# Kernel optimization log

Hardware: AMD Instinct MI355X
Metric: run time of the kernel (lower is better)

## Reference

```python
import jax, jax.numpy as jnp
import numpy as np

N_NODES = 100000
N_EDGES = 1600000
N_GRAPHS = 1000
NODES_PER_GRAPH = 100  # batch vector is arange(N)//100: exactly 100 nodes per graph
HID = 32
MAX_Z = 1000
K = 30
D_LAT = HID * 3 + 1  # 97, total_latent_dim


def setup_inputs() -> dict:
    key = jax.random.key(0)
    ks = jax.random.split(key, 24)
    s = 1.0 / np.sqrt(HID)
    inp = {
        "z": jax.random.randint(ks[0], (N_NODES,), 0, MAX_Z, dtype=jnp.int32),
        "edge_index": jax.random.randint(ks[1], (2, N_EDGES), 0, N_NODES, dtype=jnp.int32),
        "batch": (jnp.arange(N_NODES, dtype=jnp.int32) // NODES_PER_GRAPH),
        "edge_weight": jax.random.uniform(ks[2], (N_EDGES,), jnp.float32, 0.1, 1.0),
        "z_emb": jax.random.normal(ks[3], (MAX_Z, HID), jnp.float32) * 0.1,
        # GCNConv stack: [32->32, 32->32, 32->32, 32->1]
        "Wg1": jax.random.normal(ks[4], (HID, HID)) * s,
        "bg1": jnp.zeros((HID,), jnp.float32),
        "Wg2": jax.random.normal(ks[5], (HID, HID)) * s,
        "bg2": jnp.zeros((HID,), jnp.float32),
        "Wg3": jax.random.normal(ks[6], (HID, HID)) * s,
        "bg3": jnp.zeros((HID,), jnp.float32),
        "Wg4": jax.random.normal(ks[7], (HID, 1)) * s,
        "bg4": jnp.zeros((1,), jnp.float32),
        # Conv1d(1, 16, kernel=97, stride=97)
        "Wc1": jax.random.normal(ks[8], (16, D_LAT)) * (1.0 / np.sqrt(D_LAT)),
        "bc1": jnp.zeros((16,), jnp.float32),
        # Conv1d(16, 32, kernel=5, stride=1)
        "Wc2": jax.random.normal(ks[9], (32, 16, 5)) * (1.0 / np.sqrt(16 * 5)),
        "bc2": jnp.zeros((32,), jnp.float32),
        # Linear(352, 128), Linear(128, 1)
        "Wl1": jax.random.normal(ks[10], (352, 128)) * (1.0 / np.sqrt(352)),
        "bl1": jnp.zeros((128,), jnp.float32),
        "Wl2": jax.random.normal(ks[11], (128, 1)) * (1.0 / np.sqrt(128)),
        "bl2": jnp.zeros((1,), jnp.float32),
    }
    return inp


def gcn_conv(x, src, dst, ew, W, b, n):
    # PyG GCNConv: xW, add self-loops (weight 1), sym-normalize, aggregate at dst, + bias
    xw = x @ W
    deg = jax.ops.segment_sum(ew, dst, num_segments=n) + 1.0  # +1 for self loop
    dinv = jnp.where(deg > 0, jax.lax.rsqrt(deg), 0.0)
    norm = dinv[src] * ew * dinv[dst]                          # [E]
    out = jax.ops.segment_sum(norm[:, None] * xw[src], dst, num_segments=n)
    out = out + xw * (dinv * dinv)[:, None]                    # self-loop term
    return out + b


def _forward(z, edge_index, batch, edge_weight, z_emb, Wg1, bg1, Wg2, bg2, Wg3, bg3,
             Wg4, bg4, Wc1, bc1, Wc2, bc2, Wl1, bl1, Wl2, bl2):
    src, dst = edge_index[0], edge_index[1]
    n = z.shape[0]
    x = z_emb[z]                                              # [N, 32]
    xs = []
    h = x
    for W, b in ((Wg1, bg1), (Wg2, bg2), (Wg3, bg3), (Wg4, bg4)):
        h = jnp.tanh(gcn_conv(h, src, dst, edge_weight, W, b, n))
        xs.append(h)
    x = jnp.concatenate(xs, axis=-1)                          # [N, 97]
    # global_sort_pool: batch is uniform (100 nodes/graph) so dense batching is a reshape
    dense = x.reshape(N_GRAPHS, NODES_PER_GRAPH, D_LAT)       # [B, 100, 97]
    idx = jnp.argsort(-dense[:, :, -1], axis=1)[:, :K]        # sort desc by last channel
    top = jnp.take_along_axis(dense, idx[:, :, None], axis=1)  # [B, 30, 97]
    # Conv1d(1,16,97,stride=97) on flattened [B,1,30*97] == per-slot dense layer
    y = jax.nn.relu(jnp.einsum('bkd,cd->bck', top, Wc1) + bc1[None, :, None])  # [B,16,30]
    y = y.reshape(N_GRAPHS, 16, K // 2, 2).max(axis=-1)        # MaxPool1d(2,2) -> [B,16,15]
    y = jax.lax.conv_general_dilated(y, Wc2, (1,), 'VALID',
                                     dimension_numbers=('NCH', 'OIH', 'NCH'))
    y = jax.nn.relu(y + bc2[None, :, None])                    # [B,32,11]
    y = y.reshape(N_GRAPHS, -1)                                # [B,352]
    y = jax.nn.relu(y @ Wl1 + bl1)                             # dropout: eval mode, identity
    return y @ Wl2 + bl2                                       # [B,1]


def reference(z, edge_index, batch, edge_weight, z_emb, Wg1, bg1, Wg2, bg2, Wg3, bg3,
              Wg4, bg4, Wc1, bc1, Wc2, bc2, Wl1, bl1, Wl2, bl2):
    return _forward(z, edge_index, batch, edge_weight, z_emb, Wg1, bg1, Wg2, bg2, Wg3,
                    bg3, Wg4, bg4, Wc1, bc1, Wc2, bc2, Wl1, bl1, Wl2, bl2)
```

## Files before the change

kernel.cpp:

```cpp
#include <hip/hip_runtime.h>

#define HID 32
#define DLAT 97
#define NPG 100
#define TOPK 30
#define BKT_NODES 128
#define BKT_SHIFT 7
#define NBUCK 1024
#define CAPF 2432
#define CHUNK 8192

typedef float f32x4 __attribute__((ext_vector_type(4)));

__device__ __forceinline__ f32x4 gload4(const float* p) {
    f32x4 r;
    asm volatile("global_load_dwordx4 %0, %1, off" : "=v"(r) : "v"(p));
    return r;
}

__global__ __launch_bounds__(512) void binB1_kernel(
    const int* __restrict__ src, const int* __restrict__ dst,
    const float* __restrict__ ew, int* __restrict__ gcursor,
    int2* __restrict__ bedge, int E) {
    __shared__ int hist[NBUCK];
    __shared__ int lcur[NBUCK];
    __shared__ int dcache[CHUNK];
    for (int i = threadIdx.x; i < NBUCK; i += 512) hist[i] = 0;
    __syncthreads();
    int base = blockIdx.x * CHUNK;
    int M = min(E - base, CHUNK);
    for (int i = threadIdx.x; i < M; i += 512) {
        int d = dst[base + i];
        dcache[i] = d;
        atomicAdd(&hist[d >> BKT_SHIFT], 1);
    }
    __syncthreads();
    for (int b = threadIdx.x; b < NBUCK; b += 512) {
        int v = hist[b];
        lcur[b] = b * CAPF + (v ? atomicAdd(&gcursor[b], v) : 0);
    }
    __syncthreads();
    for (int i = threadIdx.x; i < M; i += 512) {
        int d = dcache[i];
        int slot = atomicAdd(&lcur[d >> BKT_SHIFT], 1);
        bedge[slot] = make_int2(src[base + i] | ((d & (BKT_NODES - 1)) << 20),
                                __float_as_int(ew[base + i]));
    }
}

__global__ __launch_bounds__(256) void scan1024_kernel(
    const int* __restrict__ g, int* __restrict__ bstart) {
    __shared__ int sh[256];
    int t = threadIdx.x;
    int t4 = t * 4;
    int a0 = g[t4], a1 = g[t4 + 1], a2 = g[t4 + 2], a3 = g[t4 + 3];
    int tsum = a0 + a1 + a2 + a3;
    sh[t] = tsum;
    __syncthreads();
    for (int off = 1; off < 256; off <<= 1) {
        int tv = (t >= off) ? sh[t - off] : 0;
        __syncthreads();
        sh[t] += tv;
        __syncthreads();
    }
    int e = sh[t] - tsum;
    bstart[t4] = e;
    bstart[t4 + 1] = e + a0;
    bstart[t4 + 2] = e + a0 + a1;
    bstart[t4 + 3] = e + a0 + a1 + a2;
}

__global__ __launch_bounds__(512) void sortlocal3_kernel(
    const int2* __restrict__ bedge, const int* __restrict__ gcursor,
    const int* __restrict__ bstart,
    const int* __restrict__ z, const float* __restrict__ z_emb,
    const float* __restrict__ W1, int2* __restrict__ csr,
    int* __restrict__ row_start, int* __restrict__ row_deg,
    float* __restrict__ dinv, float* __restrict__ xw_a, int N) {
    __shared__ int2 LDSe[CAPF];
    __shared__ int cnt[BKT_NODES];
    __shared__ int sh2[BKT_NODES];
    __shared__ int lc2[BKT_NODES];
    __shared__ int zloc[BKT_NODES];
    __shared__ float wsum[BKT_NODES];
    __shared__ float dloc[BKT_NODES];
    __shared__ float W1L[HID * HID];

    int b = blockIdx.x, t = threadIdx.x;
    for (int i = t; i < HID * HID; i += 512) W1L[i] = W1[i];
    if (t < BKT_NODES) { cnt[t] = 0; wsum[t] = 0.f; }
    __syncthreads();

    const int begOut = bstart[b];
    const int M = gcursor[b];

    for (int i = t; i < M; i += 512) {
        int2 e = bedge[(size_t)b * CAPF + i];
        LDSe[i] = e;
        int nl = (e.x >> 20) & (BKT_NODES - 1);
        atomicAdd(&cnt[nl], 1);
        atomicAdd(&wsum[nl], __int_as_float(e.y));
    }
    __syncthreads();
    int v = 0, excl = 0;
    int n = b * BKT_NODES + t;
    if (t < BKT_NODES) { v = cnt[t]; sh2[t] = v; }
    __syncthreads();
    for (int off = 1; off < BKT_NODES; off <<= 1) {
        int tv = (t >= off && t < BKT_NODES) ? sh2[t - off] : 0;
        __syncthreads();
        if (t < BKT_NODES) sh2[t] += tv;
        __syncthreads();
    }
    if (t < BKT_NODES) {
        excl = sh2[t] - v;
        lc2[t] = excl;
        float di = 1.f / sqrtf(1.f + wsum[t]);
        dloc[t] = di;
        if (n < N) {
            row_start[n] = begOut + excl;
            row_deg[n] = v;
            dinv[n] = di;
            zloc[t] = z[n];
        } else {
            zloc[t] = 0;
        }
    }
    __syncthreads();
    for (int i = t; i < M; i += 512) {
        int2 e = LDSe[i];
        int slot = atomicAdd(&lc2[(e.x >> 20) & (BKT_NODES - 1)], 1);
        csr[begOut + slot] = make_int2(e.x & 0xFFFFF, e.y);
    }
    int lim = min(BKT_NODES, N - b * BKT_NODES);
    if (lim > 0) {
        for (int idx = t; idx < lim * HID; idx += 512) {
            int nl = idx >> 5, f = idx & 31;
            const float* row = z_emb + (size_t)zloc[nl] * HID;
            float s = 0.f;
#pragma unroll
            for (int k = 0; k < HID; ++k) s += row[k] * W1L[k * HID + f];
            xw_a[(size_t)(b * BKT_NODES + nl) * HID + f] = s * dloc[nl];
        }
    }
}

template <int MODE>
__global__ __launch_bounds__(256) void agg32z_kernel(
    const int* __restrict__ row_start, const int* __restrict__ row_deg,
    const int2* __restrict__ csr, const float* __restrict__ xw,
    const float* __restrict__ b, const float* __restrict__ dinv,
    const float* __restrict__ Wn, float* __restrict__ cout,
    float* __restrict__ xw_next, int N) {
    __shared__ float WnL[HID * HID];
    int t = threadIdx.x;
    if (MODE == 0) {
        for (int i = t; i < HID * HID; i += 256) WnL[i] = Wn[i];
    } else {
        if (t < HID) WnL[t] = Wn[t];
    }
    __syncthreads();
    int tid = blockIdx.x * 256 + t;
    int n = tid >> 5;
    if (n >= N) return;
    int lane = t & 31;
    int eq = lane & 3;
    int f4 = lane & 28;
    int beg = row_start[n];
    int deg = row_deg[n];
    float di = dinv[n];
    float selfv = xw[(size_t)n * HID + lane];
    int end = beg + deg;
    float4 acc = make_float4(0.f, 0.f, 0.f, 0.f);
    for (int i = beg; i < end; i += 32) {
        int e = i + lane;
        int2 ce = csr[min(e, end - 1)];
        float we = (e < end) ? __int_as_float(ce.y) : 0.f;
        int ci = ce.x;
        int jmax = min(8, (end - i + 3) >> 2);
        f32x4 x[8];
        float w[8];
#pragma unroll
        for (int j = 0; j < 8; ++j) {
            if (j < jmax) {
                int s = 4 * j + eq;
                int idx = __shfl(ci, s, 32);
                w[j] = __shfl(we, s, 32);
                x[j] = gload4(xw + (size_t)idx * HID + f4);
            }
        }
        asm volatile("s_waitcnt vmcnt(0)" ::: "memory");
        __builtin_amdgcn_sched_barrier(0);
#pragma unroll
        for (int j = 0; j < 8; ++j) {
            if (j < jmax) {
                acc.x += w[j] * x[j].x;
                acc.y += w[j] * x[j].y;
                acc.z += w[j] * x[j].z;
                acc.w += w[j] * x[j].w;
            }
        }
    }
#pragma unroll
    for (int m = 1; m <= 2; m <<= 1) {
        acc.x += __shfl_xor(acc.x, m, 32);
        acc.y += __shfl_xor(acc.y, m, 32);
        acc.z += __shfl_xor(acc.z, m, 32);
        acc.w += __shfl_xor(acc.w, m, 32);
    }
    float s = (eq == 0) ? acc.x : (eq == 1) ? acc.y : (eq == 2) ? acc.z : acc.w;
    float outv = tanhf(di * (s + selfv) + b[lane]);
    cout[(size_t)n * HID + lane] = outv;

    if (MODE == 0) {
        float p = 0.f;
#pragma unroll
        for (int k = 0; k < HID; ++k) {
            float ok = __shfl(outv, k, 32);
            p += ok * WnL[k * HID + lane];
        }
        xw_next[(size_t)n * HID + lane] = p * di;
    } else {
        float p = outv * WnL[lane];
        p += __shfl_xor(p, 16, 32);
        p += __shfl_xor(p, 8, 32);
        p += __shfl_xor(p, 4, 32);
        p += __shfl_xor(p, 2, 32);
        p += __shfl_xor(p, 1, 32);
        if (lane == 0) xw_next[n] = p * di;
    }
}

__global__ __launch_bounds__(256) void topk_head_kernel(
    const int* __restrict__ row_start, const int* __restrict__ row_deg,
    const int2* __restrict__ csr, const float* __restrict__ xw4,
    const float* __restrict__ b4, const float* __restrict__ dinv,
    const float* __restrict__ cblk,
    const float* __restrict__ Wc1, const float* __restrict__ bc1,
    const float* __restrict__ Wc2, const float* __restrict__ bc2,
    const float* __restrict__ Wl1, const float* __restrict__ bl1,
    const float* __restrict__ Wl2, const float* __restrict__ bl2,
    float* __restrict__ out, int N) {
    int g = blockIdx.x;
    int tid = threadIdx.x;
    __shared__ float v[NPG];
    __shared__ int tidx[TOPK];
    __shared__ float tval[TOPK];
    __shared__ float top[TOPK * DLAT];
    __shared__ float Wc1L[16 * DLAT];
    __shared__ float Wc2L[32 * 16 * 5];
    __shared__ float y1[16 * TOPK];
    __shared__ float y2[16 * 15];
    __shared__ float y3[352];
    __shared__ float r[256];

    for (int i = tid; i < 16 * DLAT; i += 256) Wc1L[i] = Wc1[i];
    for (int i = tid; i < 32 * 16 * 5; i += 256) Wc2L[i] = Wc2[i];

    if (tid < NPG) {
        int n = g * NPG + tid;
        int beg = row_start[n], end = beg + row_deg[n];
        float s0 = 0.f, s1 = 0.f;
        for (int i = beg; i < end; i += 4) {
            int2 e0 = csr[min(i, end - 1)];
            int2 e1 = csr[min(i + 1, end - 1)];
            int2 e2 = csr[min(i + 2, end - 1)];
            int2 e3 = csr[min(i + 3, end - 1)];
            float x0 = xw4[e0.x], x1 = xw4[e1.x], x2 = xw4[e2.x], x3 = xw4[e3.x];
            s0 += __int_as_float(e0.y) * x0;
            if (i + 1 < end) s1 += __int_as_float(e1.y) * x1;
            if (i + 2 < end) s0 += __int_as_float(e2.y) * x2;
            if (i + 3 < end) s1 += __int_as_float(e3.y) * x3;
        }
        v[tid] = tanhf(dinv[n] * ((s0 + s1) + xw4[n]) + b4[0]);
    }
    __syncthreads();
    if (tid < NPG) {
        float vi = v[tid];
        int cnt = 0;
#pragma unroll 4
        for (int j = 0; j < NPG; ++j) {
            float vj = v[j];
            cnt += (vj > vi) || (vj == vi && j < tid);
        }
        if (cnt < TOPK) {
            tidx[cnt] = g * NPG + tid;
            tval[cnt] = vi;
        }
    }
    __syncthreads();

    for (int idx = tid; idx < TOPK * 24; idx += 256) {
        int k = idx / 24, q = idx - k * 24;
        int l = q >> 3, fq = q & 7;
        const float4 val =
            *(const float4*)(cblk + (size_t)l * N * HID + (size_t)tidx[k] * HID + fq * 4);
        float* dst = top + k * DLAT + l * HID + fq * 4;
        dst[0] = val.x; dst[1] = val.y; dst[2] = val.z; dst[3] = val.w;
    }
    if (tid < TOPK) top[tid * DLAT + 96] = tval[tid];
    __syncthreads();

    for (int idx = tid; idx < 16 * TOPK; idx += 256) {
        int c = idx / TOPK, k = idx % TOPK;
        float s = bc1[c];
        const float* w = Wc1L + c * DLAT;
        const float* t = top + k * DLAT;
#pragma unroll 4
        for (int d = 0; d < DLAT; ++d) s += t[d] * w[d];
        y1[c * TOPK + k] = fmaxf(s, 0.f);
    }
    __syncthreads();

    for (int idx = tid; idx < 16 * 15; idx += 256) {
        int c = idx / 15, j = idx % 15;
        y2[idx] = fmaxf(y1[c * TOPK + 2 * j], y1[c * TOPK + 2 * j + 1]);
    }
    __syncthreads();

    for (int idx = tid; idx < 352; idx += 256) {
        int o = idx / 11, t = idx % 11;
        float s = bc2[o];
#pragma unroll
        for (int i = 0; i < 16; ++i) {
#pragma unroll
            for (int k = 0; k < 5; ++k)
                s += Wc2L[(o * 16 + i) * 5 + k] * y2[i * 15 + t + k];
        }
        y3[idx] = fmaxf(s, 0.f);
    }
    __syncthreads();

    {
        int half = tid >> 7;
        int o = tid & 127;
        int d0 = half * 176;
        float s = (half == 0) ? bl1[o] : 0.f;
#pragma unroll 1
        for (int d = d0; d < d0 + 176; d += 8) {
            float wv[8], yv[8];
#pragma unroll
            for (int j = 0; j < 8; ++j) wv[j] = Wl1[(d + j) * 128 + o];
#pragma unroll
            for (int j = 0; j < 8; ++j) yv[j] = y3[d + j];
#pragma unroll
            for (int j = 0; j < 8; ++j) s += yv[j] * wv[j];
        }
        r[tid] = s;
    }
    __syncthreads();
    if (tid < 128) r[tid] = fmaxf(r[tid] + r[tid + 128], 0.f) * Wl2[tid];
    __syncthreads();
    if (tid < 64) r[tid] += r[tid + 64];
    __syncthreads();
    if (tid == 0) {
        float s = 0.f;
        for (int j = 0; j < 64; ++j) s += r[j];
        out[g] = s + bl2[0];
    }
}


extern "C" void kernel_launch(void* const* d_in, const int* in_sizes, int n_in,
                              void* d_out, int out_size, void* d_ws, size_t ws_size,
                              hipStream_t stream) {
    const int* z = (const int*)d_in[0];
    const int* ei = (const int*)d_in[1];
    const float* ew = (const float*)d_in[3];
    const float* z_emb = (const float*)d_in[4];
    const float* Wg[4] = {(const float*)d_in[5], (const float*)d_in[7],
                          (const float*)d_in[9], (const float*)d_in[11]};
    const float* bg[4] = {(const float*)d_in[6], (const float*)d_in[8],
                          (const float*)d_in[10], (const float*)d_in[12]};
    const float* Wc1 = (const float*)d_in[13];
    const float* bc1 = (const float*)d_in[14];
    const float* Wc2 = (const float*)d_in[15];
    const float* bc2 = (const float*)d_in[16];
    const float* Wl1 = (const float*)d_in[17];
    const float* bl1 = (const float*)d_in[18];
    const float* Wl2 = (const float*)d_in[19];
    const float* bl2 = (const float*)d_in[20];
    float* out = (float*)d_out;

    const int N = in_sizes[0];
    const int E = in_sizes[1] / 2;
    const int G = out_size;
    const int* src = ei;
    const int* dst = ei + E;

    auto cdiv = [](long long a, long long b) { return (int)((a + b - 1) / b); };
    const int NB = cdiv(E, CHUNK);
    const int NBKT = cdiv(N, BKT_NODES);

    char* ws = (char*)d_ws;
    int2* bedge = (int2*)ws;                  ws += sizeof(int2) * (size_t)NBUCK * CAPF;
    int2* csr = (int2*)ws;                    ws += sizeof(int2) * (size_t)E;
    int* gcursor = (int*)ws;                  ws += sizeof(int) * NBUCK;
    int* bstart = (int*)ws;                   ws += sizeof(int) * NBUCK;
    int* row_start = (int*)ws;                ws += sizeof(int) * N;
    int* row_deg = (int*)ws;                  ws += sizeof(int) * N;
    float* dinv = (float*)ws;                 ws += sizeof(float) * N;
    float* xw_a = (float*)ws;                 ws += sizeof(float) * (size_t)N * HID;
    float* cblk = (float*)ws;                 ws += sizeof(float) * (size_t)3 * N * HID;
    float* xw4 = (float*)ws;                  ws += sizeof(float) * N;
    float* xw_b = (float*)bedge;
    float* cb0 = cblk;
    float* cb1 = cblk + (size_t)N * HID;
    float* cb2 = cblk + (size_t)2 * N * HID;

    hipMemsetAsync(gcursor, 0, sizeof(int) * NBUCK, stream);
    binB1_kernel<<<NB, 512, 0, stream>>>(src, dst, ew, gcursor, bedge, E);
    scan1024_kernel<<<1, 256, 0, stream>>>(gcursor, bstart);
    sortlocal3_kernel<<<NBKT, 512, 0, stream>>>(bedge, gcursor, bstart, z, z_emb, Wg[0],
                                                csr, row_start, row_deg, dinv, xw_a, N);

    const int AGGB = cdiv((long long)N * 32, 256);
    agg32z_kernel<0><<<AGGB, 256, 0, stream>>>(row_start, row_deg, csr, xw_a, bg[0],
                                               dinv, Wg[1], cb0, xw_b, N);
    agg32z_kernel<0><<<AGGB, 256, 0, stream>>>(row_start, row_deg, csr, xw_b, bg[1],
                                               dinv, Wg[2], cb1, xw_a, N);
    agg32z_kernel<1><<<AGGB, 256, 0, stream>>>(row_start, row_deg, csr, xw_a, bg[2],
                                               dinv, Wg[3], cb2, xw4, N);

    topk_head_kernel<<<G, 256, 0, stream>>>(row_start, row_deg, csr, xw4, bg[3], dinv,
                                            cblk, Wc1, bc1, Wc2, bc2, Wl1, bl1,
                                            Wl2, bl2, out, N);
}
```

Baseline: 346.8 us.

## Replace bucketed two-pass CSR build with per-node histogram and atomic scatter

The CSR build no longer bins edges into fixed-capacity buckets and then sorts each bucket in LDS. It now computes per-node degree and weight sums with global atomics, scans them to get row starts, and scatters each edge directly to its slot through a per-node atomic cursor. This removes the intermediate bucket buffer and one full pass over the edges. In exchange it adds many contended global atomics (two per edge in the histogram, one per edge in the scatter), scattered writes, and nondeterministic edge order within each row.

```diff
diff --git a/kernel.cpp b/kernel.cpp
--- a/kernel.cpp
+++ b/kernel.cpp
@@ -7,7 +7,6 @@
 #define BKT_NODES 128
 #define BKT_SHIFT 7
 #define NBUCK 1024
-#define CAPF 2432
 #define CHUNK 8192
 
 typedef float f32x4 __attribute__((ext_vector_type(4)));
@@ -18,33 +17,26 @@
     return r;
 }
 
-__global__ __launch_bounds__(512) void binB1_kernel(
-    const int* __restrict__ src, const int* __restrict__ dst,
-    const float* __restrict__ ew, int* __restrict__ gcursor,
-    int2* __restrict__ bedge, int E) {
+__global__ __launch_bounds__(512) void histA_kernel(
+    const int* __restrict__ dst, const float* __restrict__ ew,
+    int* __restrict__ gcursor, int* __restrict__ deg, float* __restrict__ wsum,
+    int E) {
     __shared__ int hist[NBUCK];
-    __shared__ int lcur[NBUCK];
-    __shared__ int dcache[CHUNK];
     for (int i = threadIdx.x; i < NBUCK; i += 512) hist[i] = 0;
     __syncthreads();
     int base = blockIdx.x * CHUNK;
     int M = min(E - base, CHUNK);
     for (int i = threadIdx.x; i < M; i += 512) {
         int d = dst[base + i];
-        dcache[i] = d;
+        float w = ew[base + i];
         atomicAdd(&hist[d >> BKT_SHIFT], 1);
+        atomicAdd(&deg[d], 1);
+        atomicAdd(&wsum[d], w);
     }
     __syncthreads();
     for (int b = threadIdx.x; b < NBUCK; b += 512) {
         int v = hist[b];
-        lcur[b] = b * CAPF + (v ? atomicAdd(&gcursor[b], v) : 0);
-    }
-    __syncthreads();
-    for (int i = threadIdx.x; i < M; i += 512) {
-        int d = dcache[i];
-        int slot = atomicAdd(&lcur[d >> BKT_SHIFT], 1);
-        bedge[slot] = make_int2(src[base + i] | ((d & (BKT_NODES - 1)) << 20),
-                                __float_as_int(ew[base + i]));
+        if (v) atomicAdd(&gcursor[b], v);
     }
 }
 
@@ -70,41 +62,26 @@
     bstart[t4 + 3] = e + a0 + a1 + a2;
 }
 
-__global__ __launch_bounds__(512) void sortlocal3_kernel(
-    const int2* __restrict__ bedge, const int* __restrict__ gcursor,
+__global__ __launch_bounds__(512) void prep_kernel(
+    const int* __restrict__ deg, const float* __restrict__ wsum,
     const int* __restrict__ bstart,
     const int* __restrict__ z, const float* __restrict__ z_emb,
-    const float* __restrict__ W1, int2* __restrict__ csr,
-    int* __restrict__ row_start, int* __restrict__ row_deg,
+    const float* __restrict__ W1,
+    int* __restrict__ row_start, int* __restrict__ cursor,
     float* __restrict__ dinv, float* __restrict__ xw_a, int N) {
-    __shared__ int2 LDSe[CAPF];
-    __shared__ int cnt[BKT_NODES];
     __shared__ int sh2[BKT_NODES];
-    __shared__ int lc2[BKT_NODES];
     __shared__ int zloc[BKT_NODES];
-    __shared__ float wsum[BKT_NODES];
     __shared__ float dloc[BKT_NODES];
     __shared__ float W1L[HID * HID];
 
     int b = blockIdx.x, t = threadIdx.x;
     for (int i = t; i < HID * HID; i += 512) W1L[i] = W1[i];
-    if (t < BKT_NODES) { cnt[t] = 0; wsum[t] = 0.f; }
-    __syncthreads();
-
-    const int begOut = bstart[b];
-    const int M = gcursor[b];
-
-    for (int i = t; i < M; i += 512) {
-        int2 e = bedge[(size_t)b * CAPF + i];
-        LDSe[i] = e;
-        int nl = (e.x >> 20) & (BKT_NODES - 1);
-        atomicAdd(&cnt[nl], 1);
-        atomicAdd(&wsum[nl], __int_as_float(e.y));
-    }
-    __syncthreads();
-    int v = 0, excl = 0;
     int n = b * BKT_NODES + t;
-    if (t < BKT_NODES) { v = cnt[t]; sh2[t] = v; }
+    int v = 0;
+    if (t < BKT_NODES) {
+        v = (n < N) ? deg[n] : 0;
+        sh2[t] = v;
+    }
     __syncthreads();
     for (int off = 1; off < BKT_NODES; off <<= 1) {
         int tv = (t >= off && t < BKT_NODES) ? sh2[t - off] : 0;
@@ -113,13 +90,13 @@
         __syncthreads();
     }
     if (t < BKT_NODES) {
-        excl = sh2[t] - v;
-        lc2[t] = excl;
-        float di = 1.f / sqrtf(1.f + wsum[t]);
+        int excl = sh2[t] - v;
+        int rs = bstart[b] + excl;
+        float di = (n < N) ? 1.f / sqrtf(1.f + wsum[n]) : 0.f;
         dloc[t] = di;
         if (n < N) {
-            row_start[n] = begOut + excl;
-            row_deg[n] = v;
+            row_start[n] = rs;
+            cursor[n] = rs;
             dinv[n] = di;
             zloc[t] = z[n];
         } else {
@@ -127,11 +104,6 @@
         }
     }
     __syncthreads();
-    for (int i = t; i < M; i += 512) {
-        int2 e = LDSe[i];
-        int slot = atomicAdd(&lc2[(e.x >> 20) & (BKT_NODES - 1)], 1);
-        csr[begOut + slot] = make_int2(e.x & 0xFFFFF, e.y);
-    }
     int lim = min(BKT_NODES, N - b * BKT_NODES);
     if (lim > 0) {
         for (int idx = t; idx < lim * HID; idx += 512) {
@@ -143,6 +115,17 @@
             xw_a[(size_t)(b * BKT_NODES + nl) * HID + f] = s * dloc[nl];
         }
     }
+}
+
+__global__ __launch_bounds__(512) void scatterB_kernel(
+    const int* __restrict__ src, const int* __restrict__ dst,
+    const float* __restrict__ ew, int* __restrict__ cursor,
+    int2* __restrict__ csr, int E) {
+    int i = blockIdx.x * 512 + threadIdx.x;
+    if (i >= E) return;
+    int d = dst[i];
+    int slot = atomicAdd(&cursor[d], 1);
+    csr[slot] = make_int2(src[i], __float_as_int(ew[i]));
 }
 
 template <int MODE>
@@ -393,36 +376,38 @@
     const int NBKT = cdiv(N, BKT_NODES);
 
     char* ws = (char*)d_ws;
-    int2* bedge = (int2*)ws;                  ws += sizeof(int2) * (size_t)NBUCK * CAPF;
     int2* csr = (int2*)ws;                    ws += sizeof(int2) * (size_t)E;
+    float* cblk = (float*)ws;                 ws += sizeof(float) * (size_t)3 * N * HID;
+    float* xw_a = (float*)ws;                 ws += sizeof(float) * (size_t)N * HID;
+    float* xw_b = (float*)ws;                 ws += sizeof(float) * (size_t)N * HID;
     int* gcursor = (int*)ws;                  ws += sizeof(int) * NBUCK;
+    int* deg = (int*)ws;                      ws += sizeof(int) * N;
+    float* wsum = (float*)ws;                 ws += sizeof(float) * N;
     int* bstart = (int*)ws;                   ws += sizeof(int) * NBUCK;
     int* row_start = (int*)ws;                ws += sizeof(int) * N;
-    int* row_deg = (int*)ws;                  ws += sizeof(int) * N;
+    int* cursor = (int*)ws;                   ws += sizeof(int) * N;
     float* dinv = (float*)ws;                 ws += sizeof(float) * N;
-    float* xw_a = (float*)ws;                 ws += sizeof(float) * (size_t)N * HID;
-    float* cblk = (float*)ws;                 ws += sizeof(float) * (size_t)3 * N * HID;
     float* xw4 = (float*)ws;                  ws += sizeof(float) * N;
-    float* xw_b = (float*)bedge;
     float* cb0 = cblk;
     float* cb1 = cblk + (size_t)N * HID;
     float* cb2 = cblk + (size_t)2 * N * HID;
 
-    hipMemsetAsync(gcursor, 0, sizeof(int) * NBUCK, stream);
-    binB1_kernel<<<NB, 512, 0, stream>>>(src, dst, ew, gcursor, bedge, E);
+    hipMemsetAsync(gcursor, 0, sizeof(int) * (NBUCK + 2 * (size_t)N), stream);
+    histA_kernel<<<NB, 512, 0, stream>>>(dst, ew, gcursor, deg, wsum, E);
     scan1024_kernel<<<1, 256, 0, stream>>>(gcursor, bstart);
-    sortlocal3_kernel<<<NBKT, 512, 0, stream>>>(bedge, gcursor, bstart, z, z_emb, Wg[0],
-                                                csr, row_start, row_deg, dinv, xw_a, N);
+    prep_kernel<<<NBKT, 512, 0, stream>>>(deg, wsum, bstart, z, z_emb, Wg[0],
+                                          row_start, cursor, dinv, xw_a, N);
+    scatterB_kernel<<<cdiv(E, 512), 512, 0, stream>>>(src, dst, ew, cursor, csr, E);
 
     const int AGGB = cdiv((long long)N * 32, 256);
-    agg32z_kernel<0><<<AGGB, 256, 0, stream>>>(row_start, row_deg, csr, xw_a, bg[0],
+    agg32z_kernel<0><<<AGGB, 256, 0, stream>>>(row_start, deg, csr, xw_a, bg[0],
                                                dinv, Wg[1], cb0, xw_b, N);
-    agg32z_kernel<0><<<AGGB, 256, 0, stream>>>(row_start, row_deg, csr, xw_b, bg[1],
+    agg32z_kernel<0><<<AGGB, 256, 0, stream>>>(row_start, deg, csr, xw_b, bg[1],
                                                dinv, Wg[2], cb1, xw_a, N);
-    agg32z_kernel<1><<<AGGB, 256, 0, stream>>>(row_start, row_deg, csr, xw_a, bg[2],
+    agg32z_kernel<1><<<AGGB, 256, 0, stream>>>(row_start, deg, csr, xw_a, bg[2],
                                                dinv, Wg[3], cb2, xw4, N);
 
-    topk_head_kernel<<<G, 256, 0, stream>>>(row_start, row_deg, csr, xw4, bg[3], dinv,
+    topk_head_kernel<<<G, 256, 0, stream>>>(row_start, deg, csr, xw4, bg[3], dinv,
                                             cblk, Wc1, bc1, Wc2, bc2, Wl1, bl1,
                                             Wl2, bl2, out, N);
 }
```

Result: slower. 551.2 us (+58.9%).
